# Kernel tuning notes

Measured on AMD Instinct MI355X. Metric: run time of the kernel, lower is better.

Reference implementation:

```python
import jax, jax.numpy as jnp
import numpy as np
import math

# Config constants (from init_kwargs)
KV_CHANNELS = 128
NUM_HEADS = 32
NUM_KV_HEADS = 2
LAYER_NUMBER = 2  # apply_query_key_layer_scaling=True -> coeff = layer_number
HEAD_DIM = KV_CHANNELS
HIDDEN = KV_CHANNELS * NUM_HEADS
COEFF = float(LAYER_NUMBER)
NORM_FACTOR = math.sqrt(HEAD_DIM) * COEFF


def setup_inputs() -> dict:
    key = jax.random.key(0)
    k1, k2, k3, k4 = jax.random.split(key, 4)
    B, Q, KV = 2, 2048, 2048
    query_layer = jax.random.normal(k1, (B, NUM_HEADS, Q, HEAD_DIM), dtype=jnp.float32)
    key_layer = jax.random.normal(k2, (B, NUM_KV_HEADS, KV, HEAD_DIM), dtype=jnp.float32)
    value_layer = jax.random.normal(k3, (B, NUM_KV_HEADS, KV, HEAD_DIM), dtype=jnp.float32)
    attention_mask = jax.random.normal(k4, (B, 1, Q, KV), dtype=jnp.float32)
    return {
        "query_layer": query_layer,
        "key_layer": key_layer,
        "value_layer": value_layer,
        "attention_mask": attention_mask,
    }


def reference(query_layer, key_layer, value_layer, attention_mask):
    # Fallback (non-FusedSDPA) path of CoreAttention.forward, eval mode (no dropout).
    b, h, q_len, d = query_layer.shape
    g = key_layer.shape[1]          # num_key_value_heads
    r = h // g                      # n_rep
    # gaudi_chatglm_repeat_kv: grouped view (b, g, r, q, d) vs kv (b, g, kv, d)
    qg = query_layer.reshape(b, g, r, q_len, d)
    # scores: (b, g, r, q, kv)
    scores = jnp.einsum("bgrqd,bgkd->bgrqk", qg, key_layer) / NORM_FACTOR
    scores = scores * COEFF
    # mask unsqueezed at dim 1 -> (b, 1, 1, q, kv), broadcast-add
    scores = scores + attention_mask[:, None]
    # softmax in fp32, cast back to query dtype
    attn = jax.nn.softmax(scores.astype(jnp.float32), axis=-1).astype(query_layer.dtype)
    # AV: (b, g, r, q, d)
    out = jnp.einsum("bgrqk,bgkd->bgrqd", attn, value_layer)
    out = out.reshape(b, h, q_len, d)
    # permute (2,0,1,3) -> (q, b, h, d); reshape -> (q, b, hidden)
    context = jnp.transpose(out, (2, 0, 1, 3)).reshape(q_len, b, h * d)
    return context
```

## Files before the change

### kernel.cpp

```cpp
#include <hip/hip_runtime.h>
#include <hip/hip_bf16.h>


constexpr int Bn = 2, Hn = 32, Gn = 2, Qn = 2048, KVn = 2048, Dn = 128;
constexpr int WARPS = 4, QW = 32, QBLK = WARPS * QW;
constexpr int KVB = 32, NTILE = KVn / KVB;
constexpr float SCALE = 0.08838834764831843f;
constexpr float M0 = 16.0f;

typedef __attribute__((ext_vector_type(4))) float f32x4;
typedef __attribute__((ext_vector_type(16))) float f32x16;
typedef __attribute__((ext_vector_type(8))) __bf16 bf16x8;

__device__ __forceinline__ unsigned pk2(float a, float b) {
  union { __bf16 h[2]; unsigned u; } x;
  x.h[0] = (__bf16)a; x.h[1] = (__bf16)b;
  return x.u;
}

__global__ __launch_bounds__(256, 2)
void attn_fwd(const float* __restrict__ Qg, const float* __restrict__ Kg,
              const float* __restrict__ Vg, const float* __restrict__ Mg,
              float* __restrict__ Og) {
  __shared__ __align__(16) short Ks[2][KVB * Dn];
  __shared__ __align__(16) short Vt[2][Dn * KVB];

  const int tid = threadIdx.x;
  const int lane = tid & 63, w = tid >> 6;
  const int hi = lane >> 5, ln = lane & 31;
  const int qb = blockIdx.x * QBLK, h = blockIdx.y, b = blockIdx.z;
  const int g = h >> 4;

  const float* Qp = Qg + ((size_t)(b * Hn + h)) * Qn * Dn;
  const float* Kp = Kg + ((size_t)(b * Gn + g)) * KVn * Dn;
  const float* Vp = Vg + ((size_t)(b * Gn + g)) * KVn * Dn;

  bf16x8 aq[8];
  {
    const float* qr = Qp + (size_t)(qb + w * QW + ln) * Dn + hi * 8;
#pragma unroll
    for (int ks = 0; ks < 8; ++ks) {
      float4 f0 = *(const float4*)(qr + ks * 16);
      float4 f1 = *(const float4*)(qr + ks * 16 + 4);
      union { unsigned u[4]; bf16x8 b; } t;
      t.u[0] = pk2(f0.x, f0.y); t.u[1] = pk2(f0.z, f0.w);
      t.u[2] = pk2(f1.x, f1.y); t.u[3] = pk2(f1.z, f1.w);
      aq[ks] = t.b;
    }
  }

  const int skv = tid >> 3, sdg = tid & 7;
  const int vkp = tid >> 4, vdq = tid & 15;
  const unsigned kOff = (unsigned)(skv * (Dn * 4) + sdg * 16);
  const unsigned vOff = (unsigned)((2 * vkp) * (Dn * 4) + vdq * 32);
  const unsigned mOff = (unsigned)(((unsigned)(b * Qn + qb + w * QW + ln)) * (KVn * 4) + hi * 16);

  f32x4 kf[4], vf[4], mk[4];

  auto issueK = [&](int tile) {
    unsigned vo = kOff + (unsigned)(tile * KVB * Dn * 4);
    asm volatile("global_load_dwordx4 %0, %1, %2"            : "=v"(kf[0]) : "v"(vo), "s"(Kp));
    asm volatile("global_load_dwordx4 %0, %1, %2 offset:128" : "=v"(kf[1]) : "v"(vo), "s"(Kp));
    asm volatile("global_load_dwordx4 %0, %1, %2 offset:256" : "=v"(kf[2]) : "v"(vo), "s"(Kp));
    asm volatile("global_load_dwordx4 %0, %1, %2 offset:384" : "=v"(kf[3]) : "v"(vo), "s"(Kp));
  };
  auto issueV = [&](int tile) {
    unsigned vo = vOff + (unsigned)(tile * KVB * Dn * 4);
    asm volatile("global_load_dwordx4 %0, %1, %2"            : "=v"(vf[0]) : "v"(vo), "s"(Vp));
    asm volatile("global_load_dwordx4 %0, %1, %2 offset:16"  : "=v"(vf[1]) : "v"(vo), "s"(Vp));
    asm volatile("global_load_dwordx4 %0, %1, %2 offset:512" : "=v"(vf[2]) : "v"(vo), "s"(Vp));
    asm volatile("global_load_dwordx4 %0, %1, %2 offset:528" : "=v"(vf[3]) : "v"(vo), "s"(Vp));
  };
  auto issueM = [&](int tile) {
    unsigned vo = mOff + (unsigned)(tile * KVB * 4);
    asm volatile("global_load_dwordx4 %0, %1, %2"           : "=v"(mk[0]) : "v"(vo), "s"(Mg));
    asm volatile("global_load_dwordx4 %0, %1, %2 offset:32" : "=v"(mk[1]) : "v"(vo), "s"(Mg));
    asm volatile("global_load_dwordx4 %0, %1, %2 offset:64" : "=v"(mk[2]) : "v"(vo), "s"(Mg));
    asm volatile("global_load_dwordx4 %0, %1, %2 offset:96" : "=v"(mk[3]) : "v"(vo), "s"(Mg));
  };
  auto writeKV = [&](int buf) {
    short* ksb = Ks[buf];
    short* vtb = Vt[buf];
#pragma unroll
    for (int i = 0; i < 4; ++i) {
      unsigned w0 = pk2(kf[i][0], kf[i][1]);
      unsigned w1 = pk2(kf[i][2], kf[i][3]);
      int c = sdg * 8 + i * 64;
      int off = (skv << 8) + (c ^ ((skv & 15) << 4));
      *(uint2*)((char*)ksb + off) = make_uint2(w0, w1);
    }
#pragma unroll
    for (int j = 0; j < 8; ++j) {
      int d = vdq * 8 + j;
      float a = vf[j >> 2][j & 3];
      float bb = vf[2 + (j >> 2)][j & 3];
      int slot = (((d >> 3) ^ (d >> 1)) & 3) << 4;
      int off = (d << 6) + ((vkp * 4) ^ slot);
      *(unsigned*)((char*)vtb + off) = pk2(a, bb);
    }
  };

  f32x16 o[4];
#pragma unroll
  for (int nt = 0; nt < 4; ++nt)
#pragma unroll
    for (int e = 0; e < 16; ++e) o[nt][e] = 0.0f;
  float lsum = 0.0f;

  issueK(0); issueV(0);
  asm volatile("s_waitcnt vmcnt(0)" ::: "memory");
  asm volatile("" : "+v"(kf[0]), "+v"(kf[1]), "+v"(kf[2]), "+v"(kf[3]),
                    "+v"(vf[0]), "+v"(vf[1]), "+v"(vf[2]), "+v"(vf[3]));
  writeKV(0);
  issueM(0);
  asm volatile("s_waitcnt lgkmcnt(0)" ::: "memory");
  __builtin_amdgcn_s_barrier();

  const int ksw = (ln & 15) << 4;

  for (int t = 0; t < NTILE; ++t) {
    const int cur = t & 1;
    const int tn = (t + 1 < NTILE) ? t + 1 : t;

    issueK(tn);
    issueV(tn);

    f32x16 s;
#pragma unroll
    for (int e = 0; e < 16; ++e) s[e] = 0.0f;
    const short* ksb = Ks[cur];
    __builtin_amdgcn_s_setprio(1);
#pragma unroll
    for (int ks = 0; ks < 8; ++ks) {
      bf16x8 k0 = *(const bf16x8*)((const char*)ksb + (ln << 8) + ((ks * 32 + hi * 16) ^ ksw));
      s = __builtin_amdgcn_mfma_f32_32x32x16_bf16(k0, aq[ks], s, 0, 0, 0);
    }
    __builtin_amdgcn_s_setprio(0);

    asm volatile("s_waitcnt vmcnt(8)" ::: "memory");
    asm volatile("" : "+v"(mk[0]), "+v"(mk[1]), "+v"(mk[2]), "+v"(mk[3]));

    unsigned own[8];
    float psum = 0.0f;
#pragma unroll
    for (int gq = 0; gq < 4; ++gq) {
      float p0 = __expf(s[4 * gq + 0] * SCALE + mk[gq][0] - M0);
      float p1 = __expf(s[4 * gq + 1] * SCALE + mk[gq][1] - M0);
      float p2 = __expf(s[4 * gq + 2] * SCALE + mk[gq][2] - M0);
      float p3 = __expf(s[4 * gq + 3] * SCALE + mk[gq][3] - M0);
      psum += (p0 + p1) + (p2 + p3);
      own[2 * gq] = pk2(p0, p1);
      own[2 * gq + 1] = pk2(p2, p3);
    }
    lsum += psum;

    issueM(tn);

    unsigned sw[8];
#pragma unroll
    for (int i = 0; i < 8; ++i) sw[i] = __shfl_xor(own[i], 32);
    union Frag { unsigned u[4]; bf16x8 b; };
    Frag pf[2];
#pragma unroll
    for (int ks = 0; ks < 2; ++ks) {
      const int bsl = ks * 4;
      pf[ks].u[0] = hi ? sw[bsl + 2] : own[bsl + 0];
      pf[ks].u[1] = hi ? sw[bsl + 3] : own[bsl + 1];
      pf[ks].u[2] = hi ? own[bsl + 2] : sw[bsl + 0];
      pf[ks].u[3] = hi ? own[bsl + 3] : sw[bsl + 1];
    }

    const short* vtb = Vt[cur];
    __builtin_amdgcn_s_setprio(1);
#pragma unroll
    for (int nt = 0; nt < 4; ++nt) {
      const int d = nt * 32 + ln;
      const int swz = (((d >> 3) ^ (d >> 1)) & 3) << 4;
#pragma unroll
      for (int ks = 0; ks < 2; ++ks) {
        bf16x8 vfr = *(const bf16x8*)((const char*)vtb + (d << 6) + ((ks * 32 + hi * 16) ^ swz));
        o[nt] = __builtin_amdgcn_mfma_f32_32x32x16_bf16(vfr, pf[ks].b, o[nt], 0, 0, 0);
      }
    }
    __builtin_amdgcn_s_setprio(0);

    asm volatile("s_waitcnt vmcnt(4)" ::: "memory");
    asm volatile("" : "+v"(kf[0]), "+v"(kf[1]), "+v"(kf[2]), "+v"(kf[3]),
                      "+v"(vf[0]), "+v"(vf[1]), "+v"(vf[2]), "+v"(vf[3]));
    writeKV(cur ^ 1);
    asm volatile("s_waitcnt lgkmcnt(0)" ::: "memory");
    __builtin_amdgcn_s_barrier();
  }

  asm volatile("s_waitcnt vmcnt(0)" ::: "memory");
  asm volatile("" : "+v"(mk[0]), "+v"(mk[1]), "+v"(mk[2]), "+v"(mk[3]));

  const float ltot = lsum + __shfl_xor(lsum, 32);
  const float invl = 1.0f / ltot;
  float* outp = Og + (size_t)(qb + w * QW + ln) * (Bn * Hn * Dn) + (size_t)b * (Hn * Dn) + h * Dn;
#pragma unroll
  for (int nt = 0; nt < 4; ++nt)
#pragma unroll
    for (int gq = 0; gq < 4; ++gq) {
      float4 v;
      v.x = o[nt][gq * 4 + 0] * invl;
      v.y = o[nt][gq * 4 + 1] * invl;
      v.z = o[nt][gq * 4 + 2] * invl;
      v.w = o[nt][gq * 4 + 3] * invl;
      *(float4*)(outp + nt * 32 + gq * 8 + hi * 4) = v;
    }
}

extern "C" void kernel_launch(void* const* d_in, const int* in_sizes, int n_in,
                              void* d_out, int out_size, void* d_ws, size_t ws_size,
                              hipStream_t stream) {
  const float* q = (const float*)d_in[0];
  const float* k = (const float*)d_in[1];
  const float* v = (const float*)d_in[2];
  const float* m = (const float*)d_in[3];
  float* out = (float*)d_out;
  dim3 grid(Qn / QBLK, Hn, Bn);
  attn_fwd<<<grid, WARPS * 64, 0, stream>>>(q, k, v, m, out);
}
```

Baseline: 253.7 us.

## Prepack K/V to swizzled bf16 workspace and stage via direct global-to-LDS loads

Adds a prepack kernel that converts K and V to bf16 once per call, already in the swizzled LDS layout (V transposed). The attention kernel then copies tiles straight into shared memory with global_load_lds instead of loading fp32 into registers, converting and writing LDS in every block. This removes the repeated per-block conversion work, halves the K/V bytes read, and frees registers, which allows the launch-bound occupancy hint to rise to 3. It also rewrites the softmax exponent as exp2 with pre-folded constants, at the cost of an extra kernel launch and a workspace round trip.

```diff
diff --git a/kernel.cpp b/kernel.cpp
--- a/kernel.cpp
+++ b/kernel.cpp
@@ -7,6 +7,12 @@
 constexpr int KVB = 32, NTILE = KVn / KVB;
 constexpr float SCALE = 0.08838834764831843f;
 constexpr float M0 = 16.0f;
+constexpr float L2E = 1.4426950408889634f;
+constexpr float SCALE2 = SCALE * L2E;
+constexpr float NM0L2E = -M0 * L2E;
+
+constexpr size_t WSK_BYTES = (size_t)Bn * Gn * KVn * 256;
+constexpr size_t WSV_BYTES = (size_t)Bn * Gn * NTILE * 8192;
 
 typedef __attribute__((ext_vector_type(4))) float f32x4;
 typedef __attribute__((ext_vector_type(16))) float f32x16;
@@ -18,9 +24,33 @@
   return x.u;
 }
 
-__global__ __launch_bounds__(256, 2)
-void attn_fwd(const float* __restrict__ Qg, const float* __restrict__ Kg,
-              const float* __restrict__ Vg, const float* __restrict__ Mg,
+__global__ __launch_bounds__(256)
+void prepack(const float* __restrict__ Kg, const float* __restrict__ Vg,
+             char* __restrict__ wsK, char* __restrict__ wsV) {
+  const int i = blockIdx.x * 256 + threadIdx.x;
+  {
+    const int dp = i & 63, kv = (i >> 6) & (KVn - 1), bg = i >> 17;
+    const float* src = Kg + ((size_t)bg * KVn + kv) * Dn + 2 * dp;
+    const unsigned pr = pk2(src[0], src[1]);
+    const size_t off = (size_t)bg * (KVn * 256) + (size_t)kv * 256
+                       + ((4 * dp) ^ ((kv & 15) << 4));
+    *(unsigned*)(wsK + off) = pr;
+  }
+  {
+    const int d = i & 127, vg = (i >> 7) & 1023, bg = i >> 17;
+    const int t = vg >> 4, vkp = vg & 15;
+    const float* src = Vg + ((size_t)bg * KVn + t * KVB + 2 * vkp) * Dn + d;
+    const unsigned pr = pk2(src[0], src[Dn]);
+    const int slot = (((d >> 3) ^ (d >> 1)) & 3) << 4;
+    const size_t off = ((size_t)bg * NTILE + t) * 8192 + (d << 6)
+                       + ((vkp * 4) ^ slot);
+    *(unsigned*)(wsV + off) = pr;
+  }
+}
+
+__global__ __launch_bounds__(256, 3)
+void attn_fwd(const float* __restrict__ Qg, const float* __restrict__ Mg,
+              const char* __restrict__ wsK, const char* __restrict__ wsV,
               float* __restrict__ Og) {
   __shared__ __align__(16) short Ks[2][KVB * Dn];
   __shared__ __align__(16) short Vt[2][Dn * KVB];
@@ -29,11 +59,9 @@
   const int lane = tid & 63, w = tid >> 6;
   const int hi = lane >> 5, ln = lane & 31;
   const int qb = blockIdx.x * QBLK, h = blockIdx.y, b = blockIdx.z;
-  const int g = h >> 4;
+  const int g = h >> 4, bg = b * Gn + g;
 
   const float* Qp = Qg + ((size_t)(b * Hn + h)) * Qn * Dn;
-  const float* Kp = Kg + ((size_t)(b * Gn + g)) * KVn * Dn;
-  const float* Vp = Vg + ((size_t)(b * Gn + g)) * KVn * Dn;
 
   bf16x8 aq[8];
   {
@@ -49,28 +77,29 @@
     }
   }
 
-  const int skv = tid >> 3, sdg = tid & 7;
-  const int vkp = tid >> 4, vdq = tid & 15;
-  const unsigned kOff = (unsigned)(skv * (Dn * 4) + sdg * 16);
-  const unsigned vOff = (unsigned)((2 * vkp) * (Dn * 4) + vdq * 32);
+  const char* wsKb = wsK + (size_t)bg * (KVn * 256);
+  const char* wsVb = wsV + (size_t)bg * (NTILE * 8192);
+  auto stageKV = [&](int tile, int buf) {
+    const char* sk = wsKb + (size_t)tile * 8192 + w * 2048 + lane * 16;
+    char* dk = (char*)Ks[buf] + w * 2048;
+    __builtin_amdgcn_global_load_lds(
+        (const __attribute__((address_space(1))) void*)sk,
+        (__attribute__((address_space(3))) void*)dk, 16, 0, 0);
+    __builtin_amdgcn_global_load_lds(
+        (const __attribute__((address_space(1))) void*)(sk + 1024),
+        (__attribute__((address_space(3))) void*)(dk + 1024), 16, 0, 0);
+    const char* sv = wsVb + (size_t)tile * 8192 + w * 2048 + lane * 16;
+    char* dv = (char*)Vt[buf] + w * 2048;
+    __builtin_amdgcn_global_load_lds(
+        (const __attribute__((address_space(1))) void*)sv,
+        (__attribute__((address_space(3))) void*)dv, 16, 0, 0);
+    __builtin_amdgcn_global_load_lds(
+        (const __attribute__((address_space(1))) void*)(sv + 1024),
+        (__attribute__((address_space(3))) void*)(dv + 1024), 16, 0, 0);
+  };
+
   const unsigned mOff = (unsigned)(((unsigned)(b * Qn + qb + w * QW + ln)) * (KVn * 4) + hi * 16);
-
-  f32x4 kf[4], vf[4], mk[4];
-
-  auto issueK = [&](int tile) {
-    unsigned vo = kOff + (unsigned)(tile * KVB * Dn * 4);
-    asm volatile("global_load_dwordx4 %0, %1, %2"            : "=v"(kf[0]) : "v"(vo), "s"(Kp));
-    asm volatile("global_load_dwordx4 %0, %1, %2 offset:128" : "=v"(kf[1]) : "v"(vo), "s"(Kp));
-    asm volatile("global_load_dwordx4 %0, %1, %2 offset:256" : "=v"(kf[2]) : "v"(vo), "s"(Kp));
-    asm volatile("global_load_dwordx4 %0, %1, %2 offset:384" : "=v"(kf[3]) : "v"(vo), "s"(Kp));
-  };
-  auto issueV = [&](int tile) {
-    unsigned vo = vOff + (unsigned)(tile * KVB * Dn * 4);
-    asm volatile("global_load_dwordx4 %0, %1, %2"            : "=v"(vf[0]) : "v"(vo), "s"(Vp));
-    asm volatile("global_load_dwordx4 %0, %1, %2 offset:16"  : "=v"(vf[1]) : "v"(vo), "s"(Vp));
-    asm volatile("global_load_dwordx4 %0, %1, %2 offset:512" : "=v"(vf[2]) : "v"(vo), "s"(Vp));
-    asm volatile("global_load_dwordx4 %0, %1, %2 offset:528" : "=v"(vf[3]) : "v"(vo), "s"(Vp));
-  };
+  f32x4 mk[4];
   auto issueM = [&](int tile) {
     unsigned vo = mOff + (unsigned)(tile * KVB * 4);
     asm volatile("global_load_dwordx4 %0, %1, %2"           : "=v"(mk[0]) : "v"(vo), "s"(Mg));
@@ -78,27 +107,6 @@
     asm volatile("global_load_dwordx4 %0, %1, %2 offset:64" : "=v"(mk[2]) : "v"(vo), "s"(Mg));
     asm volatile("global_load_dwordx4 %0, %1, %2 offset:96" : "=v"(mk[3]) : "v"(vo), "s"(Mg));
   };
-  auto writeKV = [&](int buf) {
-    short* ksb = Ks[buf];
-    short* vtb = Vt[buf];
-#pragma unroll
-    for (int i = 0; i < 4; ++i) {
-      unsigned w0 = pk2(kf[i][0], kf[i][1]);
-      unsigned w1 = pk2(kf[i][2], kf[i][3]);
-      int c = sdg * 8 + i * 64;
-      int off = (skv << 8) + (c ^ ((skv & 15) << 4));
-      *(uint2*)((char*)ksb + off) = make_uint2(w0, w1);
-    }
-#pragma unroll
-    for (int j = 0; j < 8; ++j) {
-      int d = vdq * 8 + j;
-      float a = vf[j >> 2][j & 3];
-      float bb = vf[2 + (j >> 2)][j & 3];
-      int slot = (((d >> 3) ^ (d >> 1)) & 3) << 4;
-      int off = (d << 6) + ((vkp * 4) ^ slot);
-      *(unsigned*)((char*)vtb + off) = pk2(a, bb);
-    }
-  };
 
   f32x16 o[4];
 #pragma unroll
@@ -107,13 +115,9 @@
     for (int e = 0; e < 16; ++e) o[nt][e] = 0.0f;
   float lsum = 0.0f;
 
-  issueK(0); issueV(0);
-  asm volatile("s_waitcnt vmcnt(0)" ::: "memory");
-  asm volatile("" : "+v"(kf[0]), "+v"(kf[1]), "+v"(kf[2]), "+v"(kf[3]),
-                    "+v"(vf[0]), "+v"(vf[1]), "+v"(vf[2]), "+v"(vf[3]));
-  writeKV(0);
+  stageKV(0, 0);
   issueM(0);
-  asm volatile("s_waitcnt lgkmcnt(0)" ::: "memory");
+  asm volatile("s_waitcnt vmcnt(4)" ::: "memory");
   __builtin_amdgcn_s_barrier();
 
   const int ksw = (ln & 15) << 4;
@@ -122,8 +126,7 @@
     const int cur = t & 1;
     const int tn = (t + 1 < NTILE) ? t + 1 : t;
 
-    issueK(tn);
-    issueV(tn);
+    stageKV(tn, cur ^ 1);
 
     f32x16 s;
 #pragma unroll
@@ -137,17 +140,21 @@
     }
     __builtin_amdgcn_s_setprio(0);
 
-    asm volatile("s_waitcnt vmcnt(8)" ::: "memory");
+    asm volatile("s_waitcnt vmcnt(4)" ::: "memory");
     asm volatile("" : "+v"(mk[0]), "+v"(mk[1]), "+v"(mk[2]), "+v"(mk[3]));
 
     unsigned own[8];
     float psum = 0.0f;
 #pragma unroll
     for (int gq = 0; gq < 4; ++gq) {
-      float p0 = __expf(s[4 * gq + 0] * SCALE + mk[gq][0] - M0);
-      float p1 = __expf(s[4 * gq + 1] * SCALE + mk[gq][1] - M0);
-      float p2 = __expf(s[4 * gq + 2] * SCALE + mk[gq][2] - M0);
-      float p3 = __expf(s[4 * gq + 3] * SCALE + mk[gq][3] - M0);
+      float m0 = __builtin_fmaf(mk[gq][0], L2E, NM0L2E);
+      float m1 = __builtin_fmaf(mk[gq][1], L2E, NM0L2E);
+      float m2 = __builtin_fmaf(mk[gq][2], L2E, NM0L2E);
+      float m3 = __builtin_fmaf(mk[gq][3], L2E, NM0L2E);
+      float p0 = __builtin_exp2f(__builtin_fmaf(s[4 * gq + 0], SCALE2, m0));
+      float p1 = __builtin_exp2f(__builtin_fmaf(s[4 * gq + 1], SCALE2, m1));
+      float p2 = __builtin_exp2f(__builtin_fmaf(s[4 * gq + 2], SCALE2, m2));
+      float p3 = __builtin_exp2f(__builtin_fmaf(s[4 * gq + 3], SCALE2, m3));
       psum += (p0 + p1) + (p2 + p3);
       own[2 * gq] = pk2(p0, p1);
       own[2 * gq + 1] = pk2(p2, p3);
@@ -185,9 +192,6 @@
     __builtin_amdgcn_s_setprio(0);
 
     asm volatile("s_waitcnt vmcnt(4)" ::: "memory");
-    asm volatile("" : "+v"(kf[0]), "+v"(kf[1]), "+v"(kf[2]), "+v"(kf[3]),
-                      "+v"(vf[0]), "+v"(vf[1]), "+v"(vf[2]), "+v"(vf[3]));
-    writeKV(cur ^ 1);
     asm volatile("s_waitcnt lgkmcnt(0)" ::: "memory");
     __builtin_amdgcn_s_barrier();
   }
@@ -219,6 +223,10 @@
   const float* v = (const float*)d_in[2];
   const float* m = (const float*)d_in[3];
   float* out = (float*)d_out;
+  char* wsK = (char*)d_ws;
+  char* wsV = wsK + WSK_BYTES;
+
+  prepack<<<dim3((Bn * Gn * KVn * 64) / 256), 256, 0, stream>>>(k, v, wsK, wsV);
   dim3 grid(Qn / QBLK, Hn, Bn);
-  attn_fwd<<<grid, WARPS * 64, 0, stream>>>(q, k, v, m, out);
-}
+  attn_fwd<<<grid, WARPS * 64, 0, stream>>>(q, m, wsK, wsV, out);
+}
```

Measured after the change: 252.1 us. Within noise of the previous version (-0.6%).
